# Optimization experiments

Hardware: AMD Instinct MI355X
Metric: run time of the kernel (lower is better)

Reference implementation:

```python
import jax, jax.numpy as jnp
import numpy as np

IN, H, OUT = 1536, 640, 10
BATCH = 65536
KEEP = 0.1


def setup_inputs() -> dict:
    key = jax.random.key(0)
    kx, k1, k2, k3, m1, m2, m3 = jax.random.split(key, 7)
    # torch.nn.Linear-style weights: (out_features, in_features)
    W1 = jax.random.normal(k1, (H, IN), dtype=jnp.float32) * (1.0 / np.sqrt(IN))
    W2 = jax.random.normal(k2, (H, H), dtype=jnp.float32) * (1.0 / np.sqrt(H))
    W3 = jax.random.normal(k3, (OUT, H), dtype=jnp.float32) * (1.0 / np.sqrt(H))
    return {
        "x": jax.random.normal(kx, (BATCH, IN), dtype=jnp.float32),
        "W1": W1,
        "W2": W2,
        "W3": W3,
        "mask1": jax.random.bernoulli(m1, KEEP, (H, IN)),
        "mask2": jax.random.bernoulli(m2, KEEP, (H, H)),
        "mask3": jax.random.bernoulli(m3, KEEP, (OUT, H)),
    }


def reference(x, W1, W2, W3, mask1, mask2, mask3):
    w1 = jnp.where(mask1, W1, 0.0)
    w2 = jnp.where(mask2, W2, 0.0)
    w3 = jnp.where(mask3, W3, 0.0)
    h = jax.nn.gelu(x @ w1.T, approximate=False)       # [B, 640], exact GELU like F.gelu
    h = jax.nn.gelu(h @ w2.T, approximate=False)       # [B, 640]
    return h @ w3.T                                    # [B, 10]
```

## Files before the change

### kernel.cpp

```cpp
#include <hip/hip_runtime.h>
#include <hip/hip_fp16.h>
#include <math.h>

typedef _Float16 half_t;
typedef __attribute__((ext_vector_type(8))) _Float16 f16x8;
typedef __attribute__((ext_vector_type(4))) float   f32x4;
typedef __attribute__((ext_vector_type(4))) float   float4v;

#define IN_F   1536
#define HID    640
#define OUT_F  10
#define NBATCH 65536

#define SB() __builtin_amdgcn_sched_barrier(0)


__device__ __forceinline__ void gll16(const void* g, const void* l) {
    __builtin_amdgcn_global_load_lds(
        (const __attribute__((address_space(1))) unsigned*)g,
        (__attribute__((address_space(3))) unsigned*)l, 16, 0, 0);
}

__device__ __forceinline__ float gelu_fast(float z) {
    float x  = 0.70710678118654752f * z;
    float ax = fabsf(x);
    float t  = 1.0f / (1.0f + 0.3275911f * ax);
    float p  = t * (0.254829592f +
               t * (-0.284496736f +
               t * (1.421413741f +
               t * (-1.453152027f +
               t * 1.061405429f))));
    float e  = __expf(-ax * ax);
    float er = 1.0f - p * e;
    er = (x < 0.0f) ? -er : er;
    return 0.5f * z * (1.0f + er);
}


__global__ void k_detect(const unsigned* __restrict__ m, int nDwords, int* flags) {
    int f = 0, g = 0;
    for (int i = blockIdx.x * blockDim.x + threadIdx.x; i < nDwords;
         i += gridDim.x * blockDim.x) {
        unsigned d = m[i];
        f |= (d == 0x3F800000u);
        g |= (d != 0u) & (d != 1u) & (d != 0x3F800000u);
    }
    if (f) atomicOr(&flags[0], 1);
    if (g) atomicOr(&flags[1], 1);
}

__device__ __forceinline__ bool mask_at(const void* mask, int i, int isB, int isF) {
    if (isB) return ((const unsigned char*)mask)[i] != 0;
    if (isF) return ((const float*)mask)[i] != 0.0f;
    return ((const int*)mask)[i] != 0;
}

__global__ void k_mask_all(const float* __restrict__ W1, const float* __restrict__ W2,
                           const float* __restrict__ W3,
                           const void* __restrict__ m1, const void* __restrict__ m2,
                           const void* __restrict__ m3,
                           half_t* __restrict__ W1h, half_t* __restrict__ W2h,
                           float* __restrict__ W3m, const int* __restrict__ flags) {
    const int isB = flags[1], isF = flags[0];
    const int N1 = HID * IN_F, N2 = HID * HID, N3 = OUT_F * HID;
    const int NT = N1 + N2 + N3;
    for (int i = blockIdx.x * blockDim.x + threadIdx.x; i < NT;
         i += gridDim.x * blockDim.x) {
        if (i < N1) {
            W1h[i] = mask_at(m1, i, isB, isF) ? (half_t)W1[i] : (half_t)0.0f;
        } else if (i < N1 + N2) {
            int j = i - N1;
            W2h[j] = mask_at(m2, j, isB, isF) ? (half_t)W2[j] : (half_t)0.0f;
        } else {
            int j = i - N1 - N2;
            W3m[j] = mask_at(m3, j, isB, isF) ? W3[j] : 0.0f;
        }
    }
}

template <int K, bool AF32>
__global__ __launch_bounds__(512, 2) void gemm_gelu(
    const void* __restrict__ Ain, const half_t* __restrict__ Bw,
    half_t* __restrict__ Cout) {
    constexpr int NK     = K / 32;
    constexpr int ABYTES = AF32 ? 32768 : 16384;
    constexpr int SLAB   = ABYTES + 20480;
    constexpr int CL0    = AF32 ? 7 : 5;
    constexpr int CL1    = AF32 ? 6 : 4;
    static_assert(NK >= 4, "");
    __shared__ __align__(16) char lds[3 * SLAB];

    const int t = threadIdx.x, lane = t & 63, wid = t >> 6;
    const int wr = wid >> 2, wc = wid & 3;

    const int q       = (int)gridDim.x >> 3;
    const int logical = ((int)blockIdx.x & 7) * q + ((int)blockIdx.x >> 3);
    const int mb = logical >> 1, nbk = logical & 1;
    const long mBase = (long)mb * 256;
    const int  n0    = nbk * 320;

    const int rr = lane & 15, k8 = lane >> 4;
    int aBase0 = 0, aBase1 = 0, bBase = 0;
    {
        const int row = wr * 128 + rr;
        if constexpr (AF32) {
            aBase0 = row * 128 + (((2 * k8) ^ (row & 7)) << 4);
            aBase1 = aBase0 ^ 16;
        } else {
            const int ln = row >> 1;
            aBase0 = ln * 128 + ((((((row & 1) << 2) | k8)) ^ (ln & 7)) << 4);
        }
        const int nrow = wc * 80 + rr, lnb = nrow >> 1;
        bBase = ABYTES + lnb * 128 +
                ((((((nrow & 1) << 2) | k8)) ^ (lnb & 7)) << 4);
    }

    const float*  srcAf = nullptr;
    const half_t* srcAh = nullptr;
    if constexpr (AF32) {
        const int row = t >> 3, kq = (t & 7) ^ ((t >> 3) & 7);
        srcAf = (const float*)Ain + (mBase + row) * (long)K + kq * 4;
    } else {
        const int line = t >> 3, orig = (t & 7) ^ (line & 7);
        const int row = 2 * line + (orig >> 2), kq = orig & 3;
        srcAh = (const half_t*)Ain + (mBase + row) * (long)K + kq * 8;
    }
    const half_t* srcB;
    {
        const int line = t >> 3, orig = (t & 7) ^ (line & 7);
        const int nrow = 2 * line + (orig >> 2), kq = orig & 3;
        srcB = Bw + (size_t)(n0 + nrow) * K + kq * 8;
    }

    auto STAGE = [&](int k, int sb) {
        const size_t ko = (size_t)k * 32;
        if constexpr (AF32) {
#pragma unroll
            for (int r = 0; r < 4; ++r)
                gll16(srcAf + ko + (size_t)r * 64 * K,
                      &lds[sb + (t + r * 512) * 16]);
        } else {
#pragma unroll
            for (int r = 0; r < 2; ++r)
                gll16(srcAh + ko + (size_t)r * 128 * K,
                      &lds[sb + (t + r * 512) * 16]);
        }
#pragma unroll
        for (int r = 0; r < 2; ++r)
            gll16(srcB + ko + (size_t)r * 128 * K,
                  &lds[sb + ABYTES + (t + r * 512) * 16]);
        if (t < 256)
            gll16(srcB + ko + (size_t)2 * 128 * K,
                  &lds[sb + ABYTES + (t + 1024) * 16]);
    };

    f32x4 acc[8][5];
#pragma unroll
    for (int mf = 0; mf < 8; ++mf)
#pragma unroll
        for (int nf = 0; nf < 5; ++nf) {
            f32x4 z = {0.f, 0.f, 0.f, 0.f};
            acc[mf][nf] = z;
        }

    STAGE(0, 0); SB();
    STAGE(1, SLAB); SB();

    for (int ks = 0; ks < NK; ++ks) {
        if (ks + 1 < NK) {
            if (wid < 4) asm volatile("s_waitcnt vmcnt(%0)" :: "i"(CL0) : "memory");
            else         asm volatile("s_waitcnt vmcnt(%0)" :: "i"(CL1) : "memory");
        } else {
            asm volatile("s_waitcnt vmcnt(0)" ::: "memory");
        }
        __builtin_amdgcn_s_barrier();
        const int cb = (ks % 3) * SLAB;
        if (ks + 2 < NK) { STAGE(ks + 2, ((ks + 2) % 3) * SLAB); SB(); }

        f16x8 bv[5];
#pragma unroll
        for (int nf = 0; nf < 5; ++nf)
            bv[nf] = *(const f16x8*)(&lds[cb + bBase + nf * 1024]);
        f16x8 av[8];
        if constexpr (AF32) {
#pragma unroll
            for (int mf = 0; mf < 8; ++mf) {
                float4v alo = *(const float4v*)(&lds[cb + aBase0 + mf * 2048]);
                float4v ahi = *(const float4v*)(&lds[cb + aBase1 + mf * 2048]);
                f16x8 h;
#pragma unroll
                for (int i = 0; i < 4; ++i) {
                    h[i]     = (half_t)alo[i];
                    h[i + 4] = (half_t)ahi[i];
                }
                av[mf] = h;
            }
        } else {
#pragma unroll
            for (int mf = 0; mf < 8; ++mf)
                av[mf] = *(const f16x8*)(&lds[cb + aBase0 + mf * 1024]);
        }
#pragma unroll
        for (int mf = 0; mf < 8; ++mf)
#pragma unroll
            for (int nf = 0; nf < 5; ++nf)
                acc[mf][nf] = __builtin_amdgcn_mfma_f32_16x16x32_f16(
                    av[mf], bv[nf], acc[mf][nf], 0, 0, 0);
    }

    const int crow0 = (lane >> 4) * 4;
    const int ccol  = lane & 15;
#pragma unroll
    for (int mf = 0; mf < 8; ++mf)
#pragma unroll
        for (int nf = 0; nf < 5; ++nf)
#pragma unroll
            for (int j = 0; j < 4; ++j) {
                const long row = mBase + wr * 128 + mf * 16 + crow0 + j;
                const int  col = n0 + wc * 80 + nf * 16 + ccol;
                Cout[row * HID + col] = (half_t)gelu_fast(acc[mf][nf][j]);
            }
}

__global__ __launch_bounds__(256) void layer3_kernel(
    const half_t* __restrict__ h2, const float* __restrict__ W3m,
    float* __restrict__ out) {
    const int t = threadIdx.x, lane = t & 63, w = t >> 6;
    float w3r[OUT_F][10];
#pragma unroll
    for (int o = 0; o < OUT_F; ++o)
#pragma unroll
        for (int j = 0; j < 10; ++j)
            w3r[o][j] = W3m[o * HID + j * 64 + lane];

    for (long row = (long)blockIdx.x * 4 + w; row < NBATCH; row += (long)gridDim.x * 4) {
        float acc[OUT_F];
#pragma unroll
        for (int o = 0; o < OUT_F; ++o) acc[o] = 0.f;
        const half_t* hr = h2 + row * HID;
#pragma unroll
        for (int j = 0; j < 10; ++j) {
            const float h = (float)hr[j * 64 + lane];
#pragma unroll
            for (int o = 0; o < OUT_F; ++o) acc[o] += h * w3r[o][j];
        }
#pragma unroll
        for (int o = 0; o < OUT_F; ++o) {
            float v = acc[o];
#pragma unroll
            for (int off = 32; off >= 1; off >>= 1) v += __shfl_xor(v, off);
            if (lane == o) out[row * OUT_F + o] = v;
        }
    }
}


extern "C" void kernel_launch(void* const* d_in, const int* in_sizes, int n_in,
                              void* d_out, int out_size, void* d_ws, size_t ws_size,
                              hipStream_t stream) {
    const float* x  = (const float*)d_in[0];
    const float* W1 = (const float*)d_in[1];
    const float* W2 = (const float*)d_in[2];
    const float* W3 = (const float*)d_in[3];
    const void*  m1 = d_in[4];
    const void*  m2 = d_in[5];
    const void*  m3 = d_in[6];
    float* out = (float*)d_out;

    char* ws = (char*)d_ws;
    int*    flags = (int*)ws;
    half_t* W1h = (half_t*)(ws + 256);
    half_t* W2h = (half_t*)(ws + 256 + 1966080);
    float*  W3m = (float*)(ws + 256 + 1966080 + 819200);
    half_t* h1  = (half_t*)(ws + 256 + 1966080 + 819200 + 25600);
    half_t* h2  = (half_t*)((char*)h1 + (size_t)NBATCH * HID * 2);

    hipMemsetAsync(flags, 0, 8, stream);
    k_detect<<<64, 256, 0, stream>>>((const unsigned*)m1, 65536, flags);
    k_mask_all<<<1024, 256, 0, stream>>>(W1, W2, W3, m1, m2, m3, W1h, W2h, W3m, flags);

    gemm_gelu<IN_F, true><<<512, 512, 0, stream>>>((const void*)x, W1h, h1);
    gemm_gelu<HID, false><<<512, 512, 0, stream>>>((const void*)h1, W2h, h2);
    layer3_kernel<<<2048, 256, 0, stream>>>(h2, W3m, out);
}
```

Baseline: 327.7 us.

## Load weight fragments directly from global into registers, bypassing LDS

B-operand (weight) tiles are no longer staged into LDS through global_load_lds. Each wave now loads its own fragments straight from global memory into registers, double-buffered across even and odd k-steps. This shrinks the LDS footprint per slab and removes the LDS reads for B. In exchange, each of the four wave rows loads the same weight data separately (relying on L1/L2 hits), and the vmcnt wait counts change, which could hold the MFMA loop back if global latency is not hidden.

```diff
diff --git a/kernel.cpp b/kernel.cpp
--- a/kernel.cpp
+++ b/kernel.cpp
@@ -82,12 +82,10 @@
 __global__ __launch_bounds__(512, 2) void gemm_gelu(
     const void* __restrict__ Ain, const half_t* __restrict__ Bw,
     half_t* __restrict__ Cout) {
-    constexpr int NK     = K / 32;
-    constexpr int ABYTES = AF32 ? 32768 : 16384;
-    constexpr int SLAB   = ABYTES + 20480;
-    constexpr int CL0    = AF32 ? 7 : 5;
-    constexpr int CL1    = AF32 ? 6 : 4;
-    static_assert(NK >= 4, "");
+    constexpr int NK    = K / 32;
+    constexpr int SLAB  = AF32 ? 32768 : 16384;
+    constexpr int VMS   = AF32 ? 9 : 7;
+    static_assert(NK >= 4 && NK % 2 == 0, "");
     __shared__ __align__(16) char lds[3 * SLAB];
 
     const int t = threadIdx.x, lane = t & 63, wid = t >> 6;
@@ -100,7 +98,8 @@
     const int  n0    = nbk * 320;
 
     const int rr = lane & 15, k8 = lane >> 4;
-    int aBase0 = 0, aBase1 = 0, bBase = 0;
+
+    int aBase0 = 0, aBase1 = 0;
     {
         const int row = wr * 128 + rr;
         if constexpr (AF32) {
@@ -110,9 +109,6 @@
             const int ln = row >> 1;
             aBase0 = ln * 128 + ((((((row & 1) << 2) | k8)) ^ (ln & 7)) << 4);
         }
-        const int nrow = wc * 80 + rr, lnb = nrow >> 1;
-        bBase = ABYTES + lnb * 128 +
-                ((((((nrow & 1) << 2) | k8)) ^ (lnb & 7)) << 4);
     }
 
     const float*  srcAf = nullptr;
@@ -125,13 +121,6 @@
         const int row = 2 * line + (orig >> 2), kq = orig & 3;
         srcAh = (const half_t*)Ain + (mBase + row) * (long)K + kq * 8;
     }
-    const half_t* srcB;
-    {
-        const int line = t >> 3, orig = (t & 7) ^ (line & 7);
-        const int nrow = 2 * line + (orig >> 2), kq = orig & 3;
-        srcB = Bw + (size_t)(n0 + nrow) * K + kq * 8;
-    }
-
     auto STAGE = [&](int k, int sb) {
         const size_t ko = (size_t)k * 32;
         if constexpr (AF32) {
@@ -145,13 +134,14 @@
                 gll16(srcAh + ko + (size_t)r * 128 * K,
                       &lds[sb + (t + r * 512) * 16]);
         }
-#pragma unroll
-        for (int r = 0; r < 2; ++r)
-            gll16(srcB + ko + (size_t)r * 128 * K,
-                  &lds[sb + ABYTES + (t + r * 512) * 16]);
-        if (t < 256)
-            gll16(srcB + ko + (size_t)2 * 128 * K,
-                  &lds[sb + ABYTES + (t + 1024) * 16]);
+    };
+
+    const half_t* srcBf = Bw + (size_t)(n0 + wc * 80 + rr) * K + k8 * 8;
+    auto BLOAD = [&](int k, f16x8 (&bv)[5]) {
+        const half_t* p = srcBf + (size_t)k * 32;
+#pragma unroll
+        for (int nf = 0; nf < 5; ++nf)
+            bv[nf] = *(const f16x8*)(p + (size_t)nf * 16 * K);
     };
 
     f32x4 acc[8][5];
@@ -163,24 +153,22 @@
             acc[mf][nf] = z;
         }
 
+    f16x8 bvE[5], bvO[5];
+
     STAGE(0, 0); SB();
     STAGE(1, SLAB); SB();
-
-    for (int ks = 0; ks < NK; ++ks) {
-        if (ks + 1 < NK) {
-            if (wid < 4) asm volatile("s_waitcnt vmcnt(%0)" :: "i"(CL0) : "memory");
-            else         asm volatile("s_waitcnt vmcnt(%0)" :: "i"(CL1) : "memory");
-        } else {
-            asm volatile("s_waitcnt vmcnt(0)" ::: "memory");
-        }
+    BLOAD(0, bvE); SB();
+
+    auto ITER = [&](int ks, f16x8 (&bvCur)[5], f16x8 (&bvNxt)[5]) {
+        if (ks + 1 < NK)
+            asm volatile("s_waitcnt vmcnt(%0)" :: "i"(VMS) : "memory");
+        else
+            asm volatile("s_waitcnt vmcnt(5)" ::: "memory");
         __builtin_amdgcn_s_barrier();
         const int cb = (ks % 3) * SLAB;
         if (ks + 2 < NK) { STAGE(ks + 2, ((ks + 2) % 3) * SLAB); SB(); }
-
-        f16x8 bv[5];
-#pragma unroll
-        for (int nf = 0; nf < 5; ++nf)
-            bv[nf] = *(const f16x8*)(&lds[cb + bBase + nf * 1024]);
+        if (ks + 1 < NK) { BLOAD(ks + 1, bvNxt); SB(); }
+
         f16x8 av[8];
         if constexpr (AF32) {
 #pragma unroll
@@ -205,7 +193,12 @@
 #pragma unroll
             for (int nf = 0; nf < 5; ++nf)
                 acc[mf][nf] = __builtin_amdgcn_mfma_f32_16x16x32_f16(
-                    av[mf], bv[nf], acc[mf][nf], 0, 0, 0);
+                    av[mf], bvCur[nf], acc[mf][nf], 0, 0, 0);
+    };
+
+    for (int ks = 0; ks < NK; ks += 2) {
+        ITER(ks,     bvE, bvO);
+        ITER(ks + 1, bvO, bvE);
     }
 
     const int crow0 = (lane >> 4) * 4;
```

Measured after the change: 435.3 us. 32.8% more time.

## Fuse layer-3 projection into second GEMM epilogue with partial-sum reduction

Applied to the files above, without the earlier changes.

The second GEMM's epilogue now applies GELU and multiplies directly by the masked W3, reducing across lanes with shuffles. Each wave writes a per-column-slice partial result into one of 8 slices. A small final kernel sums these slices. This removes the write and re-read of the 65536x640 fp16 h2 activation and drops the separate layer-3 kernel, at the cost of more epilogue shuffles, extra registers and an 8x partial buffer.

```diff
diff --git a/kernel.cpp b/kernel.cpp
--- a/kernel.cpp
+++ b/kernel.cpp
@@ -78,10 +78,11 @@
     }
 }
 
-template <int K, bool AF32>
+template <int K, bool AF32, bool FUSE>
 __global__ __launch_bounds__(512, 2) void gemm_gelu(
     const void* __restrict__ Ain, const half_t* __restrict__ Bw,
-    half_t* __restrict__ Cout) {
+    half_t* __restrict__ Cout, const float* __restrict__ W3,
+    float* __restrict__ Pout) {
     constexpr int NK     = K / 32;
     constexpr int ABYTES = AF32 ? 32768 : 16384;
     constexpr int SLAB   = ABYTES + 20480;
@@ -100,6 +101,7 @@
     const int  n0    = nbk * 320;
 
     const int rr = lane & 15, k8 = lane >> 4;
+
     int aBase0 = 0, aBase1 = 0, bBase = 0;
     {
         const int row = wr * 128 + rr;
@@ -210,47 +212,61 @@
 
     const int crow0 = (lane >> 4) * 4;
     const int ccol  = lane & 15;
-#pragma unroll
-    for (int mf = 0; mf < 8; ++mf)
-#pragma unroll
-        for (int nf = 0; nf < 5; ++nf)
+    if constexpr (!FUSE) {
+#pragma unroll
+        for (int mf = 0; mf < 8; ++mf)
+#pragma unroll
+            for (int nf = 0; nf < 5; ++nf)
+#pragma unroll
+                for (int j = 0; j < 4; ++j) {
+                    const long row = mBase + wr * 128 + mf * 16 + crow0 + j;
+                    const int  col = n0 + wc * 80 + nf * 16 + ccol;
+                    Cout[row * HID + col] = (half_t)gelu_fast(acc[mf][nf][j]);
+                }
+    } else {
+        float w3[OUT_F][5];
+#pragma unroll
+        for (int o = 0; o < OUT_F; ++o)
+#pragma unroll
+            for (int nf = 0; nf < 5; ++nf)
+                w3[o][nf] = W3[o * HID + n0 + wc * 80 + nf * 16 + ccol];
+        float* slice = Pout + (size_t)(nbk * 4 + wc) * NBATCH * OUT_F;
+#pragma unroll
+        for (int mf = 0; mf < 8; ++mf)
 #pragma unroll
             for (int j = 0; j < 4; ++j) {
+                float p[OUT_F];
+#pragma unroll
+                for (int o = 0; o < OUT_F; ++o) p[o] = 0.f;
+#pragma unroll
+                for (int nf = 0; nf < 5; ++nf) {
+                    const float v = gelu_fast(acc[mf][nf][j]);
+#pragma unroll
+                    for (int o = 0; o < OUT_F; ++o) p[o] += v * w3[o][nf];
+                }
+#pragma unroll
+                for (int mask = 1; mask < 16; mask <<= 1)
+#pragma unroll
+                    for (int o = 0; o < OUT_F; ++o)
+                        p[o] += __shfl_xor(p[o], mask);
+                float v = 0.f;
+#pragma unroll
+                for (int o = 0; o < OUT_F; ++o) v = (ccol == o) ? p[o] : v;
                 const long row = mBase + wr * 128 + mf * 16 + crow0 + j;
-                const int  col = n0 + wc * 80 + nf * 16 + ccol;
-                Cout[row * HID + col] = (half_t)gelu_fast(acc[mf][nf][j]);
+                if (ccol < OUT_F) slice[row * OUT_F + ccol] = v;
             }
-}
-
-__global__ __launch_bounds__(256) void layer3_kernel(
-    const half_t* __restrict__ h2, const float* __restrict__ W3m,
-    float* __restrict__ out) {
-    const int t = threadIdx.x, lane = t & 63, w = t >> 6;
-    float w3r[OUT_F][10];
-#pragma unroll
-    for (int o = 0; o < OUT_F; ++o)
-#pragma unroll
-        for (int j = 0; j < 10; ++j)
-            w3r[o][j] = W3m[o * HID + j * 64 + lane];
-
-    for (long row = (long)blockIdx.x * 4 + w; row < NBATCH; row += (long)gridDim.x * 4) {
-        float acc[OUT_F];
-#pragma unroll
-        for (int o = 0; o < OUT_F; ++o) acc[o] = 0.f;
-        const half_t* hr = h2 + row * HID;
-#pragma unroll
-        for (int j = 0; j < 10; ++j) {
-            const float h = (float)hr[j * 64 + lane];
-#pragma unroll
-            for (int o = 0; o < OUT_F; ++o) acc[o] += h * w3r[o][j];
-        }
-#pragma unroll
-        for (int o = 0; o < OUT_F; ++o) {
-            float v = acc[o];
-#pragma unroll
-            for (int off = 32; off >= 1; off >>= 1) v += __shfl_xor(v, off);
-            if (lane == o) out[row * OUT_F + o] = v;
-        }
+    }
+}
+
+__global__ void k_final(const float* __restrict__ P, float* __restrict__ out) {
+    const int n = NBATCH * OUT_F;
+    for (int i = blockIdx.x * blockDim.x + threadIdx.x; i < n;
+         i += gridDim.x * blockDim.x) {
+        float s0 = P[i]                 + P[(size_t)1 * n + i];
+        float s1 = P[(size_t)2 * n + i] + P[(size_t)3 * n + i];
+        float s2 = P[(size_t)4 * n + i] + P[(size_t)5 * n + i];
+        float s3 = P[(size_t)6 * n + i] + P[(size_t)7 * n + i];
+        out[i] = (s0 + s1) + (s2 + s3);
     }
 }
 
@@ -273,13 +289,15 @@
     half_t* W2h = (half_t*)(ws + 256 + 1966080);
     float*  W3m = (float*)(ws + 256 + 1966080 + 819200);
     half_t* h1  = (half_t*)(ws + 256 + 1966080 + 819200 + 25600);
-    half_t* h2  = (half_t*)((char*)h1 + (size_t)NBATCH * HID * 2);
+    float*  Pp  = (float*)((char*)h1 + (size_t)NBATCH * HID * 2);
 
     hipMemsetAsync(flags, 0, 8, stream);
     k_detect<<<64, 256, 0, stream>>>((const unsigned*)m1, 65536, flags);
     k_mask_all<<<1024, 256, 0, stream>>>(W1, W2, W3, m1, m2, m3, W1h, W2h, W3m, flags);
 
-    gemm_gelu<IN_F, true><<<512, 512, 0, stream>>>((const void*)x, W1h, h1);
-    gemm_gelu<HID, false><<<512, 512, 0, stream>>>((const void*)h1, W2h, h2);
-    layer3_kernel<<<2048, 256, 0, stream>>>(h2, W3m, out);
-}
+    gemm_gelu<IN_F, true, false><<<512, 512, 0, stream>>>(
+        (const void*)x, W1h, h1, nullptr, nullptr);
+    gemm_gelu<HID, false, true><<<512, 512, 0, stream>>>(
+        (const void*)h1, W2h, nullptr, W3m, Pp);
+    k_final<<<1024, 256, 0, stream>>>(Pp, out);
+}
```

After: 326.7 us. About the same (-0.3%).
